# Kernel tuning notes

Hardware: AMD Instinct MI355X
Metric: run time of the kernel (lower is better)

Reference implementation:

```python
import jax, jax.numpy as jnp
import numpy as np

B, N, D_MODEL = 4, 4096, 1024
N_HEADS, D_HEAD = 16, 64
NB_FEATURES = int(D_HEAD * np.log(D_HEAD))  # 266, performer default
EPS = 1e-4


def _gaussian_orthogonal_matrix(key, m, d):
    """performer-pytorch gaussian_orthogonal_random_matrix, scaling=0."""
    n_blocks = int(np.ceil(m / d))
    keys = jax.random.split(key, n_blocks + 1)
    blocks = []
    for i in range(n_blocks):
        g = jax.random.normal(keys[i], (d, d), jnp.float32)
        q, _ = jnp.linalg.qr(g)
        blocks.append(q.T)
    mat = jnp.concatenate(blocks, axis=0)[:m]  # [m, d]
    multiplier = jnp.linalg.norm(
        jax.random.normal(keys[-1], (m, d), jnp.float32), axis=1)
    return mat * multiplier[:, None]


def setup_inputs() -> dict:
    key = jax.random.key(0)
    ks = jax.random.split(key, 7)
    s = 1.0 / np.sqrt(D_MODEL)
    x = jax.random.normal(ks[0], (B, N, D_MODEL), jnp.float32)
    Wq = jax.random.normal(ks[1], (D_MODEL, D_MODEL), jnp.float32) * s
    Wk = jax.random.normal(ks[2], (D_MODEL, D_MODEL), jnp.float32) * s
    Wv = jax.random.normal(ks[3], (D_MODEL, D_MODEL), jnp.float32) * s
    Wo = jax.random.normal(ks[4], (D_MODEL, D_MODEL), jnp.float32) * s
    bo = jnp.zeros((D_MODEL,), jnp.float32)
    proj = _gaussian_orthogonal_matrix(ks[5], NB_FEATURES, D_HEAD)
    return {"x": x, "Wq": Wq, "Wk": Wk, "Wv": Wv, "Wo": Wo, "bo": bo,
            "proj": proj}


def _softmax_kernel(data, proj, is_query):
    # data: [b, h, n, d]; proj: [m, d]  (FAVOR+ positive random features)
    ratio = proj.shape[0] ** -0.5
    dn = data.shape[-1] ** -0.25  # data_normalizer
    dash = jnp.einsum('bhnd,md->bhnm', data * dn, proj)
    diag = 0.5 * (dn ** 2) * jnp.sum(data * data, axis=-1, keepdims=True)
    if is_query:
        stab = jnp.max(dash, axis=-1, keepdims=True)
    else:
        stab = jnp.max(dash, axis=(-2, -1), keepdims=True)
    return ratio * (jnp.exp(dash - diag - stab) + EPS)


def reference(x, Wq, Wk, Wv, Wo, bo, proj):
    b, n, _ = x.shape

    def split_heads(t):  # [b,n,D] -> [b,h,n,d]
        return t.reshape(b, n, N_HEADS, D_HEAD).transpose(0, 2, 1, 3)

    q = split_heads(x @ Wq)
    k = split_heads(x @ Wk)
    v = split_heads(x @ Wv)

    qp = _softmax_kernel(q, proj, True)   # [b,h,n,m]
    kp = _softmax_kernel(k, proj, False)  # [b,h,n,m]

    # non-causal linear attention
    k_sum = jnp.sum(kp, axis=2)                                # [b,h,m]
    d_inv = 1.0 / jnp.einsum('bhnm,bhm->bhn', qp, k_sum)       # [b,h,n]
    context = jnp.einsum('bhnm,bhnd->bhmd', kp, v)             # [b,h,m,d]
    out = jnp.einsum('bhnm,bhmd,bhn->bhnd', qp, context, d_inv)

    out = out.transpose(0, 2, 1, 3).reshape(b, n, N_HEADS * D_HEAD)
    return out @ Wo + bo
```

## Files before the change

### kernel.cpp

```cpp
#include <hip/hip_runtime.h>
#include <hip/hip_bf16.h>

typedef unsigned short u16;
typedef unsigned int   u32;
typedef __bf16 bf16x8 __attribute__((ext_vector_type(8)));
typedef float  f32x4  __attribute__((ext_vector_type(4)));

#define B_    4
#define N_    4096
#define BN_   16384
#define DM_   1024
#define H_    16
#define BH_   64
#define M_    266
#define MP_   288
#define DN_    0.35355339059327373f
#define RATIO_ 0.061313933948496574f
#define EPS_   1e-4f

static __device__ __forceinline__ float b2f(u16 u) {
    union { u32 u; float f; } x; x.u = ((u32)u) << 16; return x.f;
}
static __device__ __forceinline__ u16 f2b(float f) {
    union { float f; u32 u; } x; x.f = f;
    u32 r = x.u + 0x7FFFu + ((x.u >> 16) & 1u);
    return (u16)(r >> 16);
}
static __device__ __forceinline__ u32 ford(float f) {
    u32 u = __float_as_uint(f);
    return (u & 0x80000000u) ? ~u : (u | 0x80000000u);
}
static __device__ __forceinline__ float forddec(u32 u) {
    return (u & 0x80000000u) ? __uint_as_float(u & 0x7FFFFFFFu) : __uint_as_float(~u);
}
static __device__ __forceinline__ f32x4 mfma16(bf16x8 a, bf16x8 b, f32x4 c) {
    return __builtin_amdgcn_mfma_f32_16x16x32_bf16(a, b, c, 0, 0, 0);
}
#define GLOAD16(gp, lp) __builtin_amdgcn_global_load_lds( \
    (const __attribute__((address_space(1))) void*)(gp),  \
    (__attribute__((address_space(3))) void*)(lp), 16, 0, 0)

__global__ __launch_bounds__(256) void pack_x(const float* __restrict__ x, u16* __restrict__ xb) {
    int i = (blockIdx.x * 256 + threadIdx.x) * 4;
    float4 f = *reinterpret_cast<const float4*>(x + i);
    ushort4 o;
    o.x = f2b(f.x); o.y = f2b(f.y); o.z = f2b(f.z); o.w = f2b(f.w);
    *reinterpret_cast<ushort4*>(xb + i) = o;
}

__global__ __launch_bounds__(256) void pack_w(const float* __restrict__ Wq, const float* __restrict__ Wk,
                                              const float* __restrict__ Wv, const float* __restrict__ Wo,
                                              u16* __restrict__ wT) {
    __shared__ float tile[64][65];
    int i0 = blockIdx.x * 64;
    int j0 = blockIdx.y * 64;
    const float* src = (j0 < 1024) ? Wq : (j0 < 2048) ? Wk : (j0 < 3072) ? Wv : Wo;
    int jc = j0 & 1023;
    int tr = threadIdx.x >> 6, tc = threadIdx.x & 63;
#pragma unroll
    for (int it = 0; it < 16; ++it) {
        int r = it * 4 + tr;
        tile[r][tc] = src[(size_t)(i0 + r) * 1024 + jc + tc];
    }
    __syncthreads();
#pragma unroll
    for (int it = 0; it < 16; ++it) {
        int r = it * 4 + tr;
        wT[(size_t)(j0 + r) * 1024 + i0 + tc] = f2b(tile[tc][r]);
    }
}

__global__ __launch_bounds__(256) void pack_misc(const float* __restrict__ proj, u16* __restrict__ projb,
                                                 u32* __restrict__ stabk) {
    int i = blockIdx.x * 256 + threadIdx.x;
    if (i < MP_ * 64) {
        int m = i >> 6;
        projb[i] = (m < M_) ? f2b(proj[i] * DN_) : (u16)0;
    }
    if (i < BH_) stabk[i] = 0u;
}

template<int OUTF32>
__global__ __launch_bounds__(512, 1) void gemm256(const u16* __restrict__ A, const u16* __restrict__ Bt,
                                                  void* __restrict__ C, const float* __restrict__ bias,
                                                  int Ncols, int nby) {
    __shared__ u16 As[2][256 * 64];
    __shared__ u16 Bs[2][256 * 64];
    constexpr int K = 1024, T = 16;
    int tid = threadIdx.x, lane = tid & 63, wid = tid >> 6;
    int wm = wid >> 2, wn = wid & 3;
    int lr = lane & 15, lk8 = (lane >> 4) * 8;
    int nwg = gridDim.x;
    int wg = ((int)blockIdx.x & 7) * (nwg >> 3) + (int)blockIdx.x / 8;
    int u = wg % (8 * nby), pid = wg / (8 * nby);
    size_t r0 = (size_t)(pid * 8 + (u & 7)) * 256;
    size_t c0 = (size_t)(u / 8) * 256;

    auto stage = [&](int t, int h) {
        int buf = t & 1;
        const u16* src = (h < 2) ? (A + r0 * K) : (Bt + c0 * K);
        u16* dst = (h < 2) ? As[buf] : Bs[buf];
        int rbase = (h & 1) * 128;
        int kt = t * 64;
#pragma unroll
        for (int c = 0; c < 2; ++c) {
            int li0 = rbase * 8 + c * 512 + wid * 64;
            int li = li0 + lane;
            int row = li >> 3, kk = (li & 7) * 8;
            int kks = kk ^ ((row & 7) << 3);
            GLOAD16(&src[(size_t)row * K + kt + kks], (char*)dst + (size_t)li0 * 16);
        }
    };
    auto lda = [&](int buf, int mf, int ks) {
        int row = wm * 128 + mf * 16 + lr;
        return *reinterpret_cast<const bf16x8*>(&As[buf][row * 64 + ((ks * 32 + lk8) ^ ((row & 7) << 3))]);
    };
    auto ldb = [&](int buf, int nf, int ks) {
        int row = wn * 64 + nf * 16 + lr;
        return *reinterpret_cast<const bf16x8*>(&Bs[buf][row * 64 + ((ks * 32 + lk8) ^ ((row & 7) << 3))]);
    };

    f32x4 acc[8][4] = {};
    stage(0, 0); stage(0, 1); stage(0, 2); stage(0, 3);
    stage(1, 2); stage(1, 3); stage(1, 0);
    asm volatile("s_waitcnt vmcnt(6)" ::: "memory");
    __builtin_amdgcn_s_barrier();

#pragma unroll 2
    for (int t = 0; t < T; ++t) {
        const int buf = t & 1;
        bf16x8 av[4][2], aw[4][2], bv0[2][2], bv1[2][2];
#pragma unroll
        for (int mf = 0; mf < 4; ++mf) { av[mf][0] = lda(buf, mf, 0); av[mf][1] = lda(buf, mf, 1); }
#pragma unroll
        for (int nf = 0; nf < 2; ++nf) { bv0[nf][0] = ldb(buf, nf, 0); bv0[nf][1] = ldb(buf, nf, 1); }
        if (t + 1 < T) stage(t + 1, 1);
        __builtin_amdgcn_s_barrier();
        __builtin_amdgcn_s_setprio(1);
#pragma unroll
        for (int mf = 0; mf < 4; ++mf)
#pragma unroll
            for (int nf = 0; nf < 2; ++nf) {
                acc[mf][nf] = mfma16(av[mf][0], bv0[nf][0], acc[mf][nf]);
                acc[mf][nf] = mfma16(av[mf][1], bv0[nf][1], acc[mf][nf]);
            }
        __builtin_amdgcn_s_setprio(0);
        __builtin_amdgcn_s_barrier();
#pragma unroll
        for (int nf = 0; nf < 2; ++nf) { bv1[nf][0] = ldb(buf, 2 + nf, 0); bv1[nf][1] = ldb(buf, 2 + nf, 1); }
        __builtin_amdgcn_s_barrier();
        __builtin_amdgcn_s_setprio(1);
#pragma unroll
        for (int mf = 0; mf < 4; ++mf)
#pragma unroll
            for (int nf = 0; nf < 2; ++nf) {
                acc[mf][2 + nf] = mfma16(av[mf][0], bv1[nf][0], acc[mf][2 + nf]);
                acc[mf][2 + nf] = mfma16(av[mf][1], bv1[nf][1], acc[mf][2 + nf]);
            }
        __builtin_amdgcn_s_setprio(0);
        __builtin_amdgcn_s_barrier();
#pragma unroll
        for (int mf = 0; mf < 4; ++mf) { aw[mf][0] = lda(buf, 4 + mf, 0); aw[mf][1] = lda(buf, 4 + mf, 1); }
        if (t + 2 < T) stage(t + 2, 2);
        __builtin_amdgcn_s_barrier();
        __builtin_amdgcn_s_setprio(1);
#pragma unroll
        for (int mf = 0; mf < 4; ++mf)
#pragma unroll
            for (int nf = 0; nf < 2; ++nf) {
                acc[4 + mf][nf] = mfma16(aw[mf][0], bv0[nf][0], acc[4 + mf][nf]);
                acc[4 + mf][nf] = mfma16(aw[mf][1], bv0[nf][1], acc[4 + mf][nf]);
            }
        __builtin_amdgcn_s_setprio(0);
        __builtin_amdgcn_s_barrier();
        if (t + 2 < T) { stage(t + 2, 3); stage(t + 2, 0); }
        __builtin_amdgcn_s_barrier();
        __builtin_amdgcn_s_setprio(1);
#pragma unroll
        for (int mf = 0; mf < 4; ++mf)
#pragma unroll
            for (int nf = 0; nf < 2; ++nf) {
                acc[4 + mf][2 + nf] = mfma16(aw[mf][0], bv1[nf][0], acc[4 + mf][2 + nf]);
                acc[4 + mf][2 + nf] = mfma16(aw[mf][1], bv1[nf][1], acc[4 + mf][2 + nf]);
            }
        __builtin_amdgcn_s_setprio(0);
        if (t + 2 < T) asm volatile("s_waitcnt vmcnt(6)" ::: "memory");
        else           asm volatile("s_waitcnt vmcnt(0)" ::: "memory");
        __builtin_amdgcn_s_barrier();
    }

    int rq = (lane >> 4) * 4;
#pragma unroll
    for (int mf = 0; mf < 8; ++mf)
#pragma unroll
        for (int nf = 0; nf < 4; ++nf) {
            size_t col = c0 + wn * 64 + nf * 16 + lr;
#pragma unroll
            for (int r = 0; r < 4; ++r) {
                size_t row = r0 + wm * 128 + mf * 16 + rq + r;
                float v = acc[mf][nf][r];
                if (OUTF32) reinterpret_cast<float*>(C)[row * Ncols + col] = v + bias[col];
                else        reinterpret_cast<u16*>(C)[row * Ncols + col] = f2b(v);
            }
        }
}

__global__ __launch_bounds__(256) void dashk_max(const u16* __restrict__ qkv, const u16* __restrict__ projb,
                                                 u32* __restrict__ stabk) {
    __shared__ u16 kt[128 * 64];
    __shared__ float redbuf[4];
    int bh = blockIdx.y, ch = blockIdx.x;
    int b = bh >> 4, h = bh & 15;
    const u16* src = qkv + ((size_t)(b * N_ + ch * 128)) * 3072 + 1024 + h * 64;
    int tid = threadIdx.x;
#pragma unroll
    for (int c = 0; c < 4; ++c) {
        int li = c * 256 + tid;
        int row = li >> 3, kk = (li & 7) * 8;
        *reinterpret_cast<bf16x8*>(&kt[row * 64 + (kk ^ ((row & 7) << 3))]) =
            *reinterpret_cast<const bf16x8*>(&src[(size_t)row * 3072 + kk]);
    }
    __syncthreads();
    int lane = tid & 63, wid = tid >> 6;
    int lr = lane & 15, lk8 = (lane >> 4) * 8;
    float mx = -3.0e38f;
#pragma unroll
    for (int i = 0; i < 2; ++i) {
        int row = wid * 32 + i * 16 + lr;
        bf16x8 a0 = *reinterpret_cast<const bf16x8*>(&kt[row * 64 + (lk8 ^ ((row & 7) << 3))]);
        bf16x8 a1 = *reinterpret_cast<const bf16x8*>(&kt[row * 64 + ((32 + lk8) ^ ((row & 7) << 3))]);
#pragma unroll
        for (int mf = 0; mf < 17; ++mf) {
            f32x4 d = {0.f, 0.f, 0.f, 0.f};
            const u16* pb = projb + (size_t)(mf * 16 + lr) * 64;
            d = mfma16(a0, *reinterpret_cast<const bf16x8*>(pb + lk8), d);
            d = mfma16(a1, *reinterpret_cast<const bf16x8*>(pb + 32 + lk8), d);
            if (mf * 16 + lr < M_)
                mx = fmaxf(mx, fmaxf(fmaxf(d[0], d[1]), fmaxf(d[2], d[3])));
        }
    }
#pragma unroll
    for (int off = 32; off >= 1; off >>= 1) mx = fmaxf(mx, __shfl_xor(mx, off, 64));
    if (lane == 0) redbuf[wid] = mx;
    __syncthreads();
    if (tid == 0) {
        float m = fmaxf(fmaxf(redbuf[0], redbuf[1]), fmaxf(redbuf[2], redbuf[3]));
        atomicMax(&stabk[bh], ford(m));
    }
}

__global__ __launch_bounds__(256) void kp_context(const u16* __restrict__ qkv, const u16* __restrict__ projb,
                                                  const u32* __restrict__ stabk,
                                                  float* __restrict__ ctx_part, float* __restrict__ ksum_part) {
    __shared__ u16 kt[64 * 64];
    __shared__ u16 vt[64 * 72];
    __shared__ u16 kpT[144 * 64];
    __shared__ float ksum_s[4][144];
    int bh = blockIdx.y, ch = blockIdx.x, mh = blockIdx.z;
    int b = bh >> 4, h = bh & 15;
    int tid = threadIdx.x, lane = tid & 63, wid = tid >> 6;
    int lr = lane & 15, lk8 = (lane >> 4) * 8, rq = (lane >> 4) * 4;
    float stab = forddec(stabk[bh]);
    float ksump[9];
#pragma unroll
    for (int i = 0; i < 9; ++i) ksump[i] = 0.f;
    f32x4 acc[9] = {};
    int drow = wid * 16 + lr;
    for (int sc = 0; sc < 8; ++sc) {
        int n0 = ch * 512 + sc * 64;
        const u16* srck = qkv + ((size_t)(b * N_ + n0)) * 3072 + 1024 + h * 64;
        const u16* srcv = srck + 1024;
        __syncthreads();
#pragma unroll
        for (int c = 0; c < 2; ++c) {
            int li = c * 256 + tid;
            int row = li >> 3, kk = (li & 7) * 8;
            *reinterpret_cast<bf16x8*>(&kt[row * 64 + (kk ^ ((row & 7) << 3))]) =
                *reinterpret_cast<const bf16x8*>(&srck[(size_t)row * 3072 + kk]);
            *reinterpret_cast<bf16x8*>(&vt[row * 72 + kk]) =
                *reinterpret_cast<const bf16x8*>(&srcv[(size_t)row * 3072 + kk]);
        }
        __syncthreads();
        {
            int row = wid * 16 + lr;
            bf16x8 a0 = *reinterpret_cast<const bf16x8*>(&kt[row * 64 + (lk8 ^ ((row & 7) << 3))]);
            bf16x8 a1 = *reinterpret_cast<const bf16x8*>(&kt[row * 64 + ((32 + lk8) ^ ((row & 7) << 3))]);
            float ss = 0.f;
#pragma unroll
            for (int j = 0; j < 8; ++j) {
                float f0 = (float)a0[j]; ss = fmaf(f0, f0, ss);
                float f1 = (float)a1[j]; ss = fmaf(f1, f1, ss);
            }
            ss += __shfl_xor(ss, 16, 64);
            ss += __shfl_xor(ss, 32, 64);
            float dgk[4];
#pragma unroll
            for (int r = 0; r < 4; ++r) dgk[r] = 0.0625f * __shfl(ss, rq + r, 64);
            int c4 = wid * 16 + rq;
#pragma unroll
            for (int mf = 0; mf < 9; ++mf) {
                int mfg = mh * 9 + mf;
                f32x4 d = {0.f, 0.f, 0.f, 0.f};
                const u16* pb = projb + (size_t)(mfg * 16 + lr) * 64;
                d = mfma16(a0, *reinterpret_cast<const bf16x8*>(pb + lk8), d);
                d = mfma16(a1, *reinterpret_cast<const bf16x8*>(pb + 32 + lk8), d);
                int m = mfg * 16 + lr;
                int mloc = mf * 16 + lr;
                bool real = (m < M_);
                ushort4 o;
                float v0 = real ? RATIO_ * (__expf(d[0] - dgk[0] - stab) + EPS_) : 0.f;
                float v1 = real ? RATIO_ * (__expf(d[1] - dgk[1] - stab) + EPS_) : 0.f;
                float v2 = real ? RATIO_ * (__expf(d[2] - dgk[2] - stab) + EPS_) : 0.f;
                float v3 = real ? RATIO_ * (__expf(d[3] - dgk[3] - stab) + EPS_) : 0.f;
                o.x = f2b(v0); o.y = f2b(v1); o.z = f2b(v2); o.w = f2b(v3);
                ksump[mf] += v0 + v1 + v2 + v3;
                *reinterpret_cast<ushort4*>(&kpT[mloc * 64 + (c4 ^ ((mloc & 7) << 3))]) = o;
            }
        }
        __syncthreads();
        bf16x8 bv[2];
#pragma unroll
        for (int ks = 0; ks < 2; ++ks) {
            union { u16 s[8]; bf16x8 v; } tmp;
#pragma unroll
            for (int j = 0; j < 8; ++j)
                tmp.s[j] = vt[(ks * 32 + lk8 + j) * 72 + drow];
            bv[ks] = tmp.v;
        }
#pragma unroll
        for (int ks = 0; ks < 2; ++ks) {
#pragma unroll
            for (int mf = 0; mf < 9; ++mf) {
                int mrow = mf * 16 + lr;
                bf16x8 av = *reinterpret_cast<const bf16x8*>(
                    &kpT[mrow * 64 + ((ks * 32 + lk8) ^ ((mrow & 7) << 3))]);
                acc[mf] = mfma16(av, bv[ks], acc[mf]);
            }
        }
    }
    size_t basep = ((size_t)ch * BH_ + bh) * MP_;
#pragma unroll
    for (int mf = 0; mf < 9; ++mf) {
#pragma unroll
        for (int r = 0; r < 4; ++r) {
            int m = mh * 144 + mf * 16 + rq + r;
            ctx_part[(basep + m) * 64 + wid * 16 + lr] = acc[mf][r];
        }
    }
#pragma unroll
    for (int mf = 0; mf < 9; ++mf) {
        float v = ksump[mf];
        v += __shfl_xor(v, 16, 64);
        v += __shfl_xor(v, 32, 64);
        if (lane < 16) ksum_s[wid][mf * 16 + lane] = v;
    }
    __syncthreads();
    for (int t = tid; t < 144; t += 256)
        ksum_part[basep + mh * 144 + t] = ksum_s[0][t] + ksum_s[1][t] + ksum_s[2][t] + ksum_s[3][t];
}

__global__ __launch_bounds__(256) void reduce_ctx(const float* __restrict__ ctx_part, u16* __restrict__ ctx2) {
    int t = blockIdx.x * 256 + threadIdx.x;
    int m = t % MP_;
    int rest = t / MP_;
    int d = rest & 63;
    int bh = rest >> 6;
    float s = 0.f;
#pragma unroll
    for (int c = 0; c < 8; ++c)
        s += ctx_part[(((size_t)c * BH_ + bh) * MP_ + m) * 64 + d];
    size_t idx = (((((size_t)bh * 4 + (d >> 4)) * 9 + (m >> 5)) * 64)
                  + ((m >> 3) & 3) * 16 + (d & 15)) * 8 + (m & 7);
    ctx2[idx] = f2b(s);
}

__global__ __launch_bounds__(256) void ksum_reduce(const float* __restrict__ ksum_part, float* __restrict__ ksum) {
    int t = blockIdx.x * 256 + threadIdx.x;
    float s = 0.f;
#pragma unroll
    for (int c = 0; c < 8; ++c) s += ksum_part[(size_t)c * BH_ * MP_ + t];
    ksum[t] = s;
}

__global__ __launch_bounds__(256) void qp_out(const u16* __restrict__ qkv, const u16* __restrict__ projb,
                                              const float* __restrict__ ksum,
                                              const u16* __restrict__ ctx2, u16* __restrict__ attn) {
    __shared__ u16 qt[64 * 64];
    __shared__ u16 qp_s[64 * 296];
    int bh = blockIdx.y, ch = blockIdx.x;
    int b = bh >> 4, h = bh & 15;
    int tid = threadIdx.x, lane = tid & 63, wid = tid >> 6;
    int lr = lane & 15, lk8 = (lane >> 4) * 8, rq = (lane >> 4) * 4;
    int n0 = ch * 64;
    const u16* srcq = qkv + ((size_t)(b * N_ + n0)) * 3072 + h * 64;
#pragma unroll
    for (int c = 0; c < 2; ++c) {
        int li = c * 256 + tid;
        int row = li >> 3, kk = (li & 7) * 8;
        *reinterpret_cast<bf16x8*>(&qt[row * 64 + (kk ^ ((row & 7) << 3))]) =
            *reinterpret_cast<const bf16x8*>(&srcq[(size_t)row * 3072 + kk]);
    }
    __syncthreads();
    int row = wid * 16 + lr;
    bf16x8 a0 = *reinterpret_cast<const bf16x8*>(&qt[row * 64 + (lk8 ^ ((row & 7) << 3))]);
    bf16x8 a1 = *reinterpret_cast<const bf16x8*>(&qt[row * 64 + ((32 + lk8) ^ ((row & 7) << 3))]);
    float ss = 0.f;
#pragma unroll
    for (int j = 0; j < 8; ++j) {
        float f0 = (float)a0[j]; ss = fmaf(f0, f0, ss);
        float f1 = (float)a1[j]; ss = fmaf(f1, f1, ss);
    }
    ss += __shfl_xor(ss, 16, 64);
    ss += __shfl_xor(ss, 32, 64);
    float dq[4];
#pragma unroll
    for (int r = 0; r < 4; ++r) dq[r] = 0.0625f * __shfl(ss, rq + r, 64);
    f32x4 dall[18];
    float mx[4] = {-3e38f, -3e38f, -3e38f, -3e38f};
#pragma unroll
    for (int mf = 0; mf < 18; ++mf) {
        f32x4 d = {0.f, 0.f, 0.f, 0.f};
        const u16* pb = projb + (size_t)(mf * 16 + lr) * 64;
        d = mfma16(a0, *reinterpret_cast<const bf16x8*>(pb + lk8), d);
        d = mfma16(a1, *reinterpret_cast<const bf16x8*>(pb + 32 + lk8), d);
        dall[mf] = d;
        if (mf * 16 + lr < M_) {
#pragma unroll
            for (int r = 0; r < 4; ++r) mx[r] = fmaxf(mx[r], d[r]);
        }
    }
#pragma unroll
    for (int r = 0; r < 4; ++r) {
#pragma unroll
        for (int off = 1; off < 16; off <<= 1)
            mx[r] = fmaxf(mx[r], __shfl_xor(mx[r], off, 64));
    }
    float den[4] = {0.f, 0.f, 0.f, 0.f};
#pragma unroll
    for (int mf = 0; mf < 18; ++mf) {
        int m = mf * 16 + lr;
        float ks = ksum[bh * MP_ + m];
        bool real = (m < M_);
#pragma unroll
        for (int r = 0; r < 4; ++r) {
            float qv = real ? RATIO_ * (__expf(dall[mf][r] - dq[r] - mx[r]) + EPS_) : 0.f;
            qp_s[(wid * 16 + rq + r) * 296 + m] = f2b(qv);
            den[r] = fmaf(qv, ks, den[r]);
        }
    }
    float dinv[4];
#pragma unroll
    for (int r = 0; r < 4; ++r) {
        float s = den[r];
#pragma unroll
        for (int off = 1; off < 16; off <<= 1) s += __shfl_xor(s, off, 64);
        dinv[r] = 1.0f / s;
    }
    __syncthreads();
    bf16x8 aq[9];
#pragma unroll
    for (int ks = 0; ks < 9; ++ks)
        aq[ks] = *reinterpret_cast<const bf16x8*>(&qp_s[(wid * 16 + lr) * 296 + ks * 32 + lk8]);
#pragma unroll
    for (int df = 0; df < 4; ++df) {
        f32x4 o = {0.f, 0.f, 0.f, 0.f};
        const u16* pb = ctx2 + ((((size_t)bh * 4 + df) * 9) * 64 + lane) * 8;
#pragma unroll
        for (int ks = 0; ks < 9; ++ks)
            o = mfma16(aq[ks], *reinterpret_cast<const bf16x8*>(pb + (size_t)ks * 512), o);
#pragma unroll
        for (int r = 0; r < 4; ++r) {
            size_t orow = (size_t)b * N_ + n0 + wid * 16 + rq + r;
            attn[orow * 1024 + h * 64 + df * 16 + lr] = f2b(o[r] * dinv[r]);
        }
    }
}

extern "C" void kernel_launch(void* const* d_in, const int* in_sizes, int n_in,
                              void* d_out, int out_size, void* d_ws, size_t ws_size,
                              hipStream_t stream) {
    const float* x    = (const float*)d_in[0];
    const float* Wq   = (const float*)d_in[1];
    const float* Wk   = (const float*)d_in[2];
    const float* Wv   = (const float*)d_in[3];
    const float* Wo   = (const float*)d_in[4];
    const float* bo   = (const float*)d_in[5];
    const float* proj = (const float*)d_in[6];
    char* ws = (char*)d_ws;
    u16*   xb    = (u16*)(ws + 0);
    u16*   wT    = (u16*)(ws + 33554432);
    u16*   qkv   = (u16*)(ws + 41943040);
    u16*   projb = (u16*)(ws + 142606336);
    u32*   stabk = (u32*)(ws + 144740352);
    float* ksum  = (float*)(ws + 144740608);
    u16*   ctx2  = (u16*)(ws + 144814336);
    float* ctxp  = (float*)(ws + 147173632);
    float* ksump = (float*)(ws + 184922368);
    u16*   attn  = (u16*)(ws + 185512192);
    float* out   = (float*)d_out;

    pack_x<<<16384, 256, 0, stream>>>(x, xb);
    pack_w<<<dim3(16, 64), 256, 0, stream>>>(Wq, Wk, Wv, Wo, wT);
    pack_misc<<<72, 256, 0, stream>>>(proj, projb, stabk);
    gemm256<0><<<768, 512, 0, stream>>>(xb, wT, (void*)qkv, nullptr, 3072, 12);
    dashk_max<<<dim3(32, 64), 256, 0, stream>>>(qkv, projb, stabk);
    kp_context<<<dim3(8, 64, 2), 256, 0, stream>>>(qkv, projb, stabk, ctxp, ksump);
    reduce_ctx<<<4608, 256, 0, stream>>>(ctxp, ctx2);
    ksum_reduce<<<72, 256, 0, stream>>>(ksump, ksum);
    qp_out<<<dim3(64, 64), 256, 0, stream>>>(qkv, projb, ksum, ctx2, attn);
    gemm256<1><<<256, 512, 0, stream>>>(attn, wT + 3072 * 1024, (void*)out, bo, 1024, 4);
}
```

Measured before the change: 432.6 us.

## Merge pack and reduce kernels, double-buffer K/V loads, two-tile qp_out

Result: faster. 406.5 us (-6.0%).

```diff
diff --git a/kernel.cpp b/kernel.cpp
--- a/kernel.cpp
+++ b/kernel.cpp
@@ -5,6 +5,7 @@
 typedef unsigned int   u32;
 typedef __bf16 bf16x8 __attribute__((ext_vector_type(8)));
 typedef float  f32x4  __attribute__((ext_vector_type(4)));
+typedef unsigned short u16x8 __attribute__((ext_vector_type(8)));
 
 #define B_    4
 #define N_    4096
@@ -40,44 +41,46 @@
     (const __attribute__((address_space(1))) void*)(gp),  \
     (__attribute__((address_space(3))) void*)(lp), 16, 0, 0)
 
-__global__ __launch_bounds__(256) void pack_x(const float* __restrict__ x, u16* __restrict__ xb) {
-    int i = (blockIdx.x * 256 + threadIdx.x) * 4;
-    float4 f = *reinterpret_cast<const float4*>(x + i);
-    ushort4 o;
-    o.x = f2b(f.x); o.y = f2b(f.y); o.z = f2b(f.z); o.w = f2b(f.w);
-    *reinterpret_cast<ushort4*>(xb + i) = o;
-}
-
-__global__ __launch_bounds__(256) void pack_w(const float* __restrict__ Wq, const float* __restrict__ Wk,
-                                              const float* __restrict__ Wv, const float* __restrict__ Wo,
-                                              u16* __restrict__ wT) {
+__global__ __launch_bounds__(256) void pack_all(const float* __restrict__ x, u16* __restrict__ xb,
+                                                const float* __restrict__ Wq, const float* __restrict__ Wk,
+                                                const float* __restrict__ Wv, const float* __restrict__ Wo,
+                                                u16* __restrict__ wT,
+                                                const float* __restrict__ proj, u16* __restrict__ projb,
+                                                u32* __restrict__ stabk) {
     __shared__ float tile[64][65];
-    int i0 = blockIdx.x * 64;
-    int j0 = blockIdx.y * 64;
-    const float* src = (j0 < 1024) ? Wq : (j0 < 2048) ? Wk : (j0 < 3072) ? Wv : Wo;
-    int jc = j0 & 1023;
-    int tr = threadIdx.x >> 6, tc = threadIdx.x & 63;
-#pragma unroll
-    for (int it = 0; it < 16; ++it) {
-        int r = it * 4 + tr;
-        tile[r][tc] = src[(size_t)(i0 + r) * 1024 + jc + tc];
-    }
-    __syncthreads();
-#pragma unroll
-    for (int it = 0; it < 16; ++it) {
-        int r = it * 4 + tr;
-        wT[(size_t)(j0 + r) * 1024 + i0 + tc] = f2b(tile[tc][r]);
-    }
-}
-
-__global__ __launch_bounds__(256) void pack_misc(const float* __restrict__ proj, u16* __restrict__ projb,
-                                                 u32* __restrict__ stabk) {
-    int i = blockIdx.x * 256 + threadIdx.x;
-    if (i < MP_ * 64) {
-        int m = i >> 6;
-        projb[i] = (m < M_) ? f2b(proj[i] * DN_) : (u16)0;
-    }
-    if (i < BH_) stabk[i] = 0u;
+    int bid = blockIdx.x, tid = threadIdx.x;
+    if (bid < 16384) {
+        int i = (bid * 256 + tid) * 4;
+        float4 f = *reinterpret_cast<const float4*>(x + i);
+        ushort4 o;
+        o.x = f2b(f.x); o.y = f2b(f.y); o.z = f2b(f.z); o.w = f2b(f.w);
+        *reinterpret_cast<ushort4*>(xb + i) = o;
+    } else if (bid < 16384 + 1024) {
+        int u = bid - 16384;
+        int i0 = (u & 15) * 64;
+        int j0 = (u >> 4) * 64;
+        const float* src = (j0 < 1024) ? Wq : (j0 < 2048) ? Wk : (j0 < 3072) ? Wv : Wo;
+        int jc = j0 & 1023;
+        int tr = tid >> 6, tc = tid & 63;
+#pragma unroll
+        for (int it = 0; it < 16; ++it) {
+            int r = it * 4 + tr;
+            tile[r][tc] = src[(size_t)(i0 + r) * 1024 + jc + tc];
+        }
+        __syncthreads();
+#pragma unroll
+        for (int it = 0; it < 16; ++it) {
+            int r = it * 4 + tr;
+            wT[(size_t)(j0 + r) * 1024 + i0 + tc] = f2b(tile[tc][r]);
+        }
+    } else {
+        int i = (bid - 17408) * 256 + tid;
+        if (i < MP_ * 64) {
+            int m = i >> 6;
+            projb[i] = (m < M_) ? f2b(proj[i] * DN_) : (u16)0;
+        }
+        if (i < BH_) stabk[i] = 0u;
+    }
 }
 
 template<int OUTF32>
@@ -129,33 +132,20 @@
 #pragma unroll 2
     for (int t = 0; t < T; ++t) {
         const int buf = t & 1;
-        bf16x8 av[4][2], aw[4][2], bv0[2][2], bv1[2][2];
+        bf16x8 av[4][2], aw[4][2], bv[4][2];
 #pragma unroll
         for (int mf = 0; mf < 4; ++mf) { av[mf][0] = lda(buf, mf, 0); av[mf][1] = lda(buf, mf, 1); }
 #pragma unroll
-        for (int nf = 0; nf < 2; ++nf) { bv0[nf][0] = ldb(buf, nf, 0); bv0[nf][1] = ldb(buf, nf, 1); }
+        for (int nf = 0; nf < 4; ++nf) { bv[nf][0] = ldb(buf, nf, 0); bv[nf][1] = ldb(buf, nf, 1); }
         if (t + 1 < T) stage(t + 1, 1);
         __builtin_amdgcn_s_barrier();
         __builtin_amdgcn_s_setprio(1);
 #pragma unroll
         for (int mf = 0; mf < 4; ++mf)
 #pragma unroll
-            for (int nf = 0; nf < 2; ++nf) {
-                acc[mf][nf] = mfma16(av[mf][0], bv0[nf][0], acc[mf][nf]);
-                acc[mf][nf] = mfma16(av[mf][1], bv0[nf][1], acc[mf][nf]);
-            }
-        __builtin_amdgcn_s_setprio(0);
-        __builtin_amdgcn_s_barrier();
-#pragma unroll
-        for (int nf = 0; nf < 2; ++nf) { bv1[nf][0] = ldb(buf, 2 + nf, 0); bv1[nf][1] = ldb(buf, 2 + nf, 1); }
-        __builtin_amdgcn_s_barrier();
-        __builtin_amdgcn_s_setprio(1);
-#pragma unroll
-        for (int mf = 0; mf < 4; ++mf)
-#pragma unroll
-            for (int nf = 0; nf < 2; ++nf) {
-                acc[mf][2 + nf] = mfma16(av[mf][0], bv1[nf][0], acc[mf][2 + nf]);
-                acc[mf][2 + nf] = mfma16(av[mf][1], bv1[nf][1], acc[mf][2 + nf]);
+            for (int nf = 0; nf < 4; ++nf) {
+                acc[mf][nf] = mfma16(av[mf][0], bv[nf][0], acc[mf][nf]);
+                acc[mf][nf] = mfma16(av[mf][1], bv[nf][1], acc[mf][nf]);
             }
         __builtin_amdgcn_s_setprio(0);
         __builtin_amdgcn_s_barrier();
@@ -168,8 +158,8 @@
         for (int mf = 0; mf < 4; ++mf)
 #pragma unroll
             for (int nf = 0; nf < 2; ++nf) {
-                acc[4 + mf][nf] = mfma16(aw[mf][0], bv0[nf][0], acc[4 + mf][nf]);
-                acc[4 + mf][nf] = mfma16(aw[mf][1], bv0[nf][1], acc[4 + mf][nf]);
+                acc[4 + mf][nf] = mfma16(aw[mf][0], bv[nf][0], acc[4 + mf][nf]);
+                acc[4 + mf][nf] = mfma16(aw[mf][1], bv[nf][1], acc[4 + mf][nf]);
             }
         __builtin_amdgcn_s_setprio(0);
         __builtin_amdgcn_s_barrier();
@@ -180,8 +170,8 @@
         for (int mf = 0; mf < 4; ++mf)
 #pragma unroll
             for (int nf = 0; nf < 2; ++nf) {
-                acc[4 + mf][2 + nf] = mfma16(aw[mf][0], bv1[nf][0], acc[4 + mf][2 + nf]);
-                acc[4 + mf][2 + nf] = mfma16(aw[mf][1], bv1[nf][1], acc[4 + mf][2 + nf]);
+                acc[4 + mf][2 + nf] = mfma16(aw[mf][0], bv[2 + nf][0], acc[4 + mf][2 + nf]);
+                acc[4 + mf][2 + nf] = mfma16(aw[mf][1], bv[2 + nf][1], acc[4 + mf][2 + nf]);
             }
         __builtin_amdgcn_s_setprio(0);
         if (t + 2 < T) asm volatile("s_waitcnt vmcnt(6)" ::: "memory");
@@ -252,8 +242,8 @@
 __global__ __launch_bounds__(256) void kp_context(const u16* __restrict__ qkv, const u16* __restrict__ projb,
                                                   const u32* __restrict__ stabk,
                                                   float* __restrict__ ctx_part, float* __restrict__ ksum_part) {
-    __shared__ u16 kt[64 * 64];
-    __shared__ u16 vt[64 * 72];
+    __shared__ u16 kt[2][64 * 64];
+    __shared__ u16 vt[2][64 * 64];
     __shared__ u16 kpT[144 * 64];
     __shared__ float ksum_s[4][144];
     int bh = blockIdx.y, ch = blockIdx.x, mh = blockIdx.z;
@@ -266,25 +256,33 @@
     for (int i = 0; i < 9; ++i) ksump[i] = 0.f;
     f32x4 acc[9] = {};
     int drow = wid * 16 + lr;
-    for (int sc = 0; sc < 8; ++sc) {
+
+    auto stage_kv = [&](int sc, int buf) {
         int n0 = ch * 512 + sc * 64;
         const u16* srck = qkv + ((size_t)(b * N_ + n0)) * 3072 + 1024 + h * 64;
         const u16* srcv = srck + 1024;
-        __syncthreads();
-#pragma unroll
-        for (int c = 0; c < 2; ++c) {
-            int li = c * 256 + tid;
+#pragma unroll
+        for (int p = 0; p < 2; ++p) {
+            int li0 = (wid * 2 + p) * 64;
+            int li = li0 + lane;
             int row = li >> 3, kk = (li & 7) * 8;
-            *reinterpret_cast<bf16x8*>(&kt[row * 64 + (kk ^ ((row & 7) << 3))]) =
-                *reinterpret_cast<const bf16x8*>(&srck[(size_t)row * 3072 + kk]);
-            *reinterpret_cast<bf16x8*>(&vt[row * 72 + kk]) =
-                *reinterpret_cast<const bf16x8*>(&srcv[(size_t)row * 3072 + kk]);
-        }
-        __syncthreads();
+            int kks = kk ^ ((row & 7) << 3);
+            GLOAD16(&srck[(size_t)row * 3072 + kks], (char*)kt[buf] + (size_t)li0 * 16);
+            GLOAD16(&srcv[(size_t)row * 3072 + kks], (char*)vt[buf] + (size_t)li0 * 16);
+        }
+    };
+
+    stage_kv(0, 0);
+    asm volatile("s_waitcnt vmcnt(0)" ::: "memory");
+    for (int sc = 0; sc < 8; ++sc) {
+        int buf = sc & 1;
+        __builtin_amdgcn_s_barrier();
+        if (sc < 7) stage_kv(sc + 1, buf ^ 1);
+        int n0 = ch * 512 + sc * 64;
         {
             int row = wid * 16 + lr;
-            bf16x8 a0 = *reinterpret_cast<const bf16x8*>(&kt[row * 64 + (lk8 ^ ((row & 7) << 3))]);
-            bf16x8 a1 = *reinterpret_cast<const bf16x8*>(&kt[row * 64 + ((32 + lk8) ^ ((row & 7) << 3))]);
+            bf16x8 a0 = *reinterpret_cast<const bf16x8*>(&kt[buf][row * 64 + (lk8 ^ ((row & 7) << 3))]);
+            bf16x8 a1 = *reinterpret_cast<const bf16x8*>(&kt[buf][row * 64 + ((32 + lk8) ^ ((row & 7) << 3))]);
             float ss = 0.f;
 #pragma unroll
             for (int j = 0; j < 8; ++j) {
@@ -317,14 +315,17 @@
                 *reinterpret_cast<ushort4*>(&kpT[mloc * 64 + (c4 ^ ((mloc & 7) << 3))]) = o;
             }
         }
-        __syncthreads();
+        asm volatile("s_waitcnt lgkmcnt(0)" ::: "memory");
+        __builtin_amdgcn_s_barrier();
         bf16x8 bv[2];
 #pragma unroll
         for (int ks = 0; ks < 2; ++ks) {
             union { u16 s[8]; bf16x8 v; } tmp;
 #pragma unroll
-            for (int j = 0; j < 8; ++j)
-                tmp.s[j] = vt[(ks * 32 + lk8 + j) * 72 + drow];
+            for (int j = 0; j < 8; ++j) {
+                int n = ks * 32 + lk8 + j;
+                tmp.s[j] = vt[buf][n * 64 + ((drow & ~7) ^ ((n & 7) << 3)) + (drow & 7)];
+            }
             bv[ks] = tmp.v;
         }
 #pragma unroll
@@ -337,6 +338,7 @@
                 acc[mf] = mfma16(av, bv[ks], acc[mf]);
             }
         }
+        if (sc < 7) asm volatile("s_waitcnt vmcnt(0)" ::: "memory");
     }
     size_t basep = ((size_t)ch * BH_ + bh) * MP_;
 #pragma unroll
@@ -359,27 +361,36 @@
         ksum_part[basep + mh * 144 + t] = ksum_s[0][t] + ksum_s[1][t] + ksum_s[2][t] + ksum_s[3][t];
 }
 
-__global__ __launch_bounds__(256) void reduce_ctx(const float* __restrict__ ctx_part, u16* __restrict__ ctx2) {
-    int t = blockIdx.x * 256 + threadIdx.x;
-    int m = t % MP_;
-    int rest = t / MP_;
-    int d = rest & 63;
-    int bh = rest >> 6;
-    float s = 0.f;
-#pragma unroll
-    for (int c = 0; c < 8; ++c)
-        s += ctx_part[(((size_t)c * BH_ + bh) * MP_ + m) * 64 + d];
-    size_t idx = (((((size_t)bh * 4 + (d >> 4)) * 9 + (m >> 5)) * 64)
-                  + ((m >> 3) & 3) * 16 + (d & 15)) * 8 + (m & 7);
-    ctx2[idx] = f2b(s);
-}
-
-__global__ __launch_bounds__(256) void ksum_reduce(const float* __restrict__ ksum_part, float* __restrict__ ksum) {
-    int t = blockIdx.x * 256 + threadIdx.x;
-    float s = 0.f;
-#pragma unroll
-    for (int c = 0; c < 8; ++c) s += ksum_part[(size_t)c * BH_ * MP_ + t];
-    ksum[t] = s;
+__global__ __launch_bounds__(256) void reduce_all(const float* __restrict__ ctx_part,
+                                                  const float* __restrict__ ksum_part,
+                                                  u16* __restrict__ ctx2, float* __restrict__ ksum) {
+    int bid = blockIdx.x, tid = threadIdx.x;
+    if (bid < 576) {
+        int t = bid * 256 + tid;
+        int mo = t % 36;
+        int rest = t / 36;
+        int d = rest & 63;
+        int bh = rest >> 6;
+        u16x8 o;
+#pragma unroll
+        for (int mm = 0; mm < 8; ++mm) {
+            int m = mo * 8 + mm;
+            float s = 0.f;
+#pragma unroll
+            for (int c = 0; c < 8; ++c)
+                s += ctx_part[(((size_t)c * BH_ + bh) * MP_ + m) * 64 + d];
+            o[mm] = f2b(s);
+        }
+        size_t idx = ((((size_t)bh * 4 + (d >> 4)) * 9 + (mo >> 2)) * 64
+                      + (mo & 3) * 16 + (d & 15)) * 8;
+        *reinterpret_cast<u16x8*>(ctx2 + idx) = o;
+    } else {
+        int t = (bid - 576) * 256 + tid;
+        float s = 0.f;
+#pragma unroll
+        for (int c = 0; c < 8; ++c) s += ksum_part[(size_t)c * BH_ * MP_ + t];
+        ksum[t] = s;
+    }
 }
 
 __global__ __launch_bounds__(256) void qp_out(const u16* __restrict__ qkv, const u16* __restrict__ projb,
@@ -391,87 +402,109 @@
     int b = bh >> 4, h = bh & 15;
     int tid = threadIdx.x, lane = tid & 63, wid = tid >> 6;
     int lr = lane & 15, lk8 = (lane >> 4) * 8, rq = (lane >> 4) * 4;
-    int n0 = ch * 64;
-    const u16* srcq = qkv + ((size_t)(b * N_ + n0)) * 3072 + h * 64;
+    float ksh[18];
+#pragma unroll
+    for (int mf = 0; mf < 18; ++mf) ksh[mf] = ksum[bh * MP_ + mf * 16 + lr];
+    const u16* srcq = qkv + ((size_t)(b * N_ + ch * 128)) * 3072 + h * 64;
+    int srow = tid >> 2, skk = (tid & 3) * 16;
+    int ssw = (srow & 7) << 3;
+    int sd0 = srow * 64 + (skk ^ ssw);
+    int sd1 = srow * 64 + ((skk + 8) ^ ssw);
+    {
+        u16x8 qa = *reinterpret_cast<const u16x8*>(&srcq[(size_t)srow * 3072 + skk]);
+        u16x8 qb = *reinterpret_cast<const u16x8*>(&srcq[(size_t)srow * 3072 + skk + 8]);
+        *reinterpret_cast<u16x8*>(&qt[sd0]) = qa;
+        *reinterpret_cast<u16x8*>(&qt[sd1]) = qb;
+    }
+    asm volatile("s_waitcnt lgkmcnt(0)" ::: "memory");
+    __builtin_amdgcn_s_barrier();
 #pragma unroll
     for (int c = 0; c < 2; ++c) {
-        int li = c * 256 + tid;
-        int row = li >> 3, kk = (li & 7) * 8;
-        *reinterpret_cast<bf16x8*>(&qt[row * 64 + (kk ^ ((row & 7) << 3))]) =
-            *reinterpret_cast<const bf16x8*>(&srcq[(size_t)row * 3072 + kk]);
-    }
-    __syncthreads();
-    int row = wid * 16 + lr;
-    bf16x8 a0 = *reinterpret_cast<const bf16x8*>(&qt[row * 64 + (lk8 ^ ((row & 7) << 3))]);
-    bf16x8 a1 = *reinterpret_cast<const bf16x8*>(&qt[row * 64 + ((32 + lk8) ^ ((row & 7) << 3))]);
-    float ss = 0.f;
-#pragma unroll
-    for (int j = 0; j < 8; ++j) {
-        float f0 = (float)a0[j]; ss = fmaf(f0, f0, ss);
-        float f1 = (float)a1[j]; ss = fmaf(f1, f1, ss);
-    }
-    ss += __shfl_xor(ss, 16, 64);
-    ss += __shfl_xor(ss, 32, 64);
-    float dq[4];
-#pragma unroll
-    for (int r = 0; r < 4; ++r) dq[r] = 0.0625f * __shfl(ss, rq + r, 64);
-    f32x4 dall[18];
-    float mx[4] = {-3e38f, -3e38f, -3e38f, -3e38f};
-#pragma unroll
-    for (int mf = 0; mf < 18; ++mf) {
-        f32x4 d = {0.f, 0.f, 0.f, 0.f};
-        const u16* pb = projb + (size_t)(mf * 16 + lr) * 64;
-        d = mfma16(a0, *reinterpret_cast<const bf16x8*>(pb + lk8), d);
-        d = mfma16(a1, *reinterpret_cast<const bf16x8*>(pb + 32 + lk8), d);
-        dall[mf] = d;
-        if (mf * 16 + lr < M_) {
-#pragma unroll
-            for (int r = 0; r < 4; ++r) mx[r] = fmaxf(mx[r], d[r]);
-        }
-    }
-#pragma unroll
-    for (int r = 0; r < 4; ++r) {
-#pragma unroll
-        for (int off = 1; off < 16; off <<= 1)
-            mx[r] = fmaxf(mx[r], __shfl_xor(mx[r], off, 64));
-    }
-    float den[4] = {0.f, 0.f, 0.f, 0.f};
-#pragma unroll
-    for (int mf = 0; mf < 18; ++mf) {
-        int m = mf * 16 + lr;
-        float ks = ksum[bh * MP_ + m];
-        bool real = (m < M_);
+        int n0 = ch * 128 + c * 64;
+        int row = wid * 16 + lr;
+        bf16x8 a0 = *reinterpret_cast<const bf16x8*>(&qt[row * 64 + (lk8 ^ ((row & 7) << 3))]);
+        bf16x8 a1 = *reinterpret_cast<const bf16x8*>(&qt[row * 64 + ((32 + lk8) ^ ((row & 7) << 3))]);
+        u16x8 qa, qb;
+        if (c == 0) {
+            qa = *reinterpret_cast<const u16x8*>(&srcq[(size_t)(64 + srow) * 3072 + skk]);
+            qb = *reinterpret_cast<const u16x8*>(&srcq[(size_t)(64 + srow) * 3072 + skk + 8]);
+        }
+        float ss = 0.f;
+#pragma unroll
+        for (int j = 0; j < 8; ++j) {
+            float f0 = (float)a0[j]; ss = fmaf(f0, f0, ss);
+            float f1 = (float)a1[j]; ss = fmaf(f1, f1, ss);
+        }
+        ss += __shfl_xor(ss, 16, 64);
+        ss += __shfl_xor(ss, 32, 64);
+        float dq[4];
+#pragma unroll
+        for (int r = 0; r < 4; ++r) dq[r] = 0.0625f * __shfl(ss, rq + r, 64);
+        f32x4 dall[18];
+        float mx[4] = {-3e38f, -3e38f, -3e38f, -3e38f};
+#pragma unroll
+        for (int mf = 0; mf < 18; ++mf) {
+            f32x4 d = {0.f, 0.f, 0.f, 0.f};
+            const u16* pb = projb + (size_t)(mf * 16 + lr) * 64;
+            d = mfma16(a0, *reinterpret_cast<const bf16x8*>(pb + lk8), d);
+            d = mfma16(a1, *reinterpret_cast<const bf16x8*>(pb + 32 + lk8), d);
+            dall[mf] = d;
+            if (mf * 16 + lr < M_) {
+#pragma unroll
+                for (int r = 0; r < 4; ++r) mx[r] = fmaxf(mx[r], d[r]);
+            }
+        }
 #pragma unroll
         for (int r = 0; r < 4; ++r) {
-            float qv = real ? RATIO_ * (__expf(dall[mf][r] - dq[r] - mx[r]) + EPS_) : 0.f;
-            qp_s[(wid * 16 + rq + r) * 296 + m] = f2b(qv);
-            den[r] = fmaf(qv, ks, den[r]);
-        }
-    }
-    float dinv[4];
-#pragma unroll
-    for (int r = 0; r < 4; ++r) {
-        float s = den[r];
-#pragma unroll
-        for (int off = 1; off < 16; off <<= 1) s += __shfl_xor(s, off, 64);
-        dinv[r] = 1.0f / s;
-    }
-    __syncthreads();
-    bf16x8 aq[9];
-#pragma unroll
-    for (int ks = 0; ks < 9; ++ks)
-        aq[ks] = *reinterpret_cast<const bf16x8*>(&qp_s[(wid * 16 + lr) * 296 + ks * 32 + lk8]);
-#pragma unroll
-    for (int df = 0; df < 4; ++df) {
-        f32x4 o = {0.f, 0.f, 0.f, 0.f};
-        const u16* pb = ctx2 + ((((size_t)bh * 4 + df) * 9) * 64 + lane) * 8;
+#pragma unroll
+            for (int off = 1; off < 16; off <<= 1)
+                mx[r] = fmaxf(mx[r], __shfl_xor(mx[r], off, 64));
+        }
+        float den[4] = {0.f, 0.f, 0.f, 0.f};
+#pragma unroll
+        for (int mf = 0; mf < 18; ++mf) {
+            int m = mf * 16 + lr;
+            bool real = (m < M_);
+#pragma unroll
+            for (int r = 0; r < 4; ++r) {
+                float qv = real ? RATIO_ * (__expf(dall[mf][r] - dq[r] - mx[r]) + EPS_) : 0.f;
+                qp_s[(wid * 16 + rq + r) * 296 + m] = f2b(qv);
+                den[r] = fmaf(qv, ksh[mf], den[r]);
+            }
+        }
+        float dinv[4];
+#pragma unroll
+        for (int r = 0; r < 4; ++r) {
+            float s = den[r];
+#pragma unroll
+            for (int off = 1; off < 16; off <<= 1) s += __shfl_xor(s, off, 64);
+            dinv[r] = 1.0f / s;
+        }
+        __builtin_amdgcn_s_barrier();
+        if (c == 0) {
+            *reinterpret_cast<u16x8*>(&qt[sd0]) = qa;
+            *reinterpret_cast<u16x8*>(&qt[sd1]) = qb;
+        }
+        bf16x8 aq[9];
 #pragma unroll
         for (int ks = 0; ks < 9; ++ks)
-            o = mfma16(aq[ks], *reinterpret_cast<const bf16x8*>(pb + (size_t)ks * 512), o);
-#pragma unroll
-        for (int r = 0; r < 4; ++r) {
-            size_t orow = (size_t)b * N_ + n0 + wid * 16 + rq + r;
-            attn[orow * 1024 + h * 64 + df * 16 + lr] = f2b(o[r] * dinv[r]);
+            aq[ks] = *reinterpret_cast<const bf16x8*>(&qp_s[(wid * 16 + lr) * 296 + ks * 32 + lk8]);
+#pragma unroll
+        for (int df = 0; df < 4; ++df) {
+            f32x4 o = {0.f, 0.f, 0.f, 0.f};
+            const u16* pb = ctx2 + ((((size_t)bh * 4 + df) * 9) * 64 + lane) * 8;
+#pragma unroll
+            for (int ks = 0; ks < 9; ++ks)
+                o = mfma16(aq[ks], *reinterpret_cast<const bf16x8*>(pb + (size_t)ks * 512), o);
+#pragma unroll
+            for (int r = 0; r < 4; ++r) {
+                size_t orow = (size_t)b * N_ + n0 + wid * 16 + rq + r;
+                attn[orow * 1024 + h * 64 + df * 16 + lr] = f2b(o[r] * dinv[r]);
+            }
+        }
+        if (c == 0) {
+            asm volatile("s_waitcnt lgkmcnt(0)" ::: "memory");
+            __builtin_amdgcn_s_barrier();
         }
     }
 }
@@ -499,14 +532,11 @@
     u16*   attn  = (u16*)(ws + 185512192);
     float* out   = (float*)d_out;
 
-    pack_x<<<16384, 256, 0, stream>>>(x, xb);
-    pack_w<<<dim3(16, 64), 256, 0, stream>>>(Wq, Wk, Wv, Wo, wT);
-    pack_misc<<<72, 256, 0, stream>>>(proj, projb, stabk);
+    pack_all<<<17480, 256, 0, stream>>>(x, xb, Wq, Wk, Wv, Wo, wT, proj, projb, stabk);
     gemm256<0><<<768, 512, 0, stream>>>(xb, wT, (void*)qkv, nullptr, 3072, 12);
     dashk_max<<<dim3(32, 64), 256, 0, stream>>>(qkv, projb, stabk);
     kp_context<<<dim3(8, 64, 2), 256, 0, stream>>>(qkv, projb, stabk, ctxp, ksump);
-    reduce_ctx<<<4608, 256, 0, stream>>>(ctxp, ctx2);
-    ksum_reduce<<<72, 256, 0, stream>>>(ksump, ksum);
-    qp_out<<<dim3(64, 64), 256, 0, stream>>>(qkv, projb, ksum, ctx2, attn);
+    reduce_all<<<648, 256, 0, stream>>>(ctxp, ksump, ctx2, ksum);
+    qp_out<<<dim3(32, 64), 256, 0, stream>>>(qkv, projb, ksum, ctx2, attn);
     gemm256<1><<<256, 512, 0, stream>>>(attn, wT + 3072 * 1024, (void*)out, bo, 1024, 4);
 }
```
